# Kernel optimization log

Hardware: AMD Instinct MI355X
Metric: run time of the kernel (lower is better)

The kernel has to match this reference:

```python
import jax, jax.numpy as jnp
import numpy as np

B, T, C = 2, 2048, 1024
H = 16
HD = C // H  # head_dim = 64
SCALE = HD ** -0.5

def setup_inputs() -> dict:
    key = jax.random.key(0)
    ks = jax.random.split(key, 5)
    s = 1.0 / np.sqrt(C)
    return {
        "x": jax.random.normal(ks[0], (B, T, C), dtype=jnp.float32),
        "Wq": jax.random.normal(ks[1], (C, C), dtype=jnp.float32) * s,
        "Wk": jax.random.normal(ks[2], (C, C), dtype=jnp.float32) * s,
        "Wv": jax.random.normal(ks[3], (C, C), dtype=jnp.float32) * s,
        "Wp": jax.random.normal(ks[4], (C, C), dtype=jnp.float32) * s,
        "bp": jnp.zeros((C,), dtype=jnp.float32),
    }

def reference(x, Wq, Wk, Wv, Wp, bp):
    b, t, c = x.shape
    # QKV projections (no bias, qkv_bias=False) -> [B,T,H,HD]
    q = (x @ Wq).reshape(b, t, H, HD)
    k = (x @ Wk).reshape(b, t, H, HD)
    v = (x @ Wv).reshape(b, t, H, HD)
    # scores [B,H,T,T]
    scores = jnp.einsum("bqhd,bkhd->bhqk", q, k) * SCALE
    causal = jnp.tril(jnp.ones((t, t), dtype=bool))
    scores = jnp.where(causal, scores, -jnp.inf)
    attn = jax.nn.softmax(scores, axis=-1)  # dropout = identity (eval mode)
    out = jnp.einsum("bhqk,bkhd->bqhd", attn, v).reshape(b, t, c)
    return out @ Wp + bp
```

## Files before the change

### kernel.cpp

```cpp
#include <hip/hip_runtime.h>


typedef __attribute__((ext_vector_type(8))) short shortx8;
typedef __attribute__((ext_vector_type(4))) short shortx4;
typedef __attribute__((ext_vector_type(8))) unsigned short ushortx8;
typedef __attribute__((ext_vector_type(4))) float f32x4;
typedef __attribute__((ext_vector_type(16))) float f32x16;

#define MFMA16(a, b, c) __builtin_amdgcn_mfma_f32_16x16x32_bf16((a), (b), (c), 0, 0, 0)
#define MFMA32(a, b, c) __builtin_amdgcn_mfma_f32_32x32x16_bf16((a), (b), (c), 0, 0, 0)

#define SC_L2E 0.18033688011112042f

__device__ __forceinline__ unsigned short f2bf(float f) {
  union { float f; unsigned u; } v; v.f = f;
  unsigned r = v.u + 0x7fffu + ((v.u >> 16) & 1u);
  return (unsigned short)(r >> 16);
}

__device__ __forceinline__ unsigned cvtpk(float a, float b) {
  unsigned r;
  asm("v_cvt_pk_bf16_f32 %0, %1, %2" : "=v"(r) : "v"(a), "v"(b));
  return r;
}

__device__ __forceinline__ float fexp2(float x) {
#if __has_builtin(__builtin_amdgcn_exp2f)
  return __builtin_amdgcn_exp2f(x);
#else
  return exp2f(x);
#endif
}

__device__ __forceinline__ void gload16(const void* g, void* l) {
  __builtin_amdgcn_global_load_lds(
      (const __attribute__((address_space(1))) void*)g,
      (__attribute__((address_space(3))) void*)l, 16, 0, 0);
}

__global__ __launch_bounds__(256) void cvt_x(const float* __restrict__ x,
                                             unsigned short* __restrict__ xb, int n4) {
  int i = blockIdx.x * 256 + threadIdx.x;
  if (i < n4) {
    float4 v = ((const float4*)x)[i];
    unsigned short* o = xb + (size_t)i * 4;
    o[0] = f2bf(v.x); o[1] = f2bf(v.y); o[2] = f2bf(v.z); o[3] = f2bf(v.w);
  }
}

__global__ __launch_bounds__(256) void transpose_w4(
    const float* __restrict__ Wq, const float* __restrict__ Wk,
    const float* __restrict__ Wv, const float* __restrict__ Wp,
    unsigned short* __restrict__ wqkvT, unsigned short* __restrict__ wpT) {
  __shared__ float tile[32][33];
  const int zi = blockIdx.z;
  const float* src = (zi == 0) ? Wq : (zi == 1) ? Wk : (zi == 2) ? Wv : Wp;
  unsigned short* dst = (zi == 3) ? wpT : wqkvT + (size_t)zi * 1048576;
  const int bx = blockIdx.x * 32, by = blockIdx.y * 32;
  const int tx = threadIdx.x & 31, ty = threadIdx.x >> 5;
  #pragma unroll
  for (int i = 0; i < 32; i += 8)
    tile[ty + i][tx] = src[(size_t)(by + ty + i) * 1024 + bx + tx];
  __syncthreads();
  #pragma unroll
  for (int i = 0; i < 32; i += 8)
    dst[(size_t)(bx + ty + i) * 1024 + by + tx] = f2bf(tile[tx][ty + i]);
}

__global__ __launch_bounds__(256) void gemm_bt(
    const unsigned short* __restrict__ A, const unsigned short* __restrict__ BT,
    unsigned short* __restrict__ Cb, float* __restrict__ Cf,
    const float* __restrict__ bias, int M, int N, int K,
    float qscale, int scale_cols, unsigned short* __restrict__ vTo) {
  __shared__ unsigned short As[2][128 * 32];
  __shared__ unsigned short Bs[2][128 * 32];
  const int tid = threadIdx.x;
  const int lane = tid & 63, w = tid >> 6;
  const int wr = w >> 1, wc = w & 1;
  const int brow = blockIdx.y << 7, bcol = blockIdx.x << 7;

  f32x4 z = {0.f, 0.f, 0.f, 0.f};
  f32x4 acc[4][4];
  #pragma unroll
  for (int m = 0; m < 4; ++m)
    #pragma unroll
    for (int n = 0; n < 4; ++n) acc[m][n] = z;

  const int srow = tid >> 2;
  const int scol = (tid & 3) << 3;
  const unsigned short* Ap = A + (size_t)(brow + srow) * K + scol;
  const unsigned short* Bp = BT + (size_t)(bcol + srow) * K + scol;
  const size_t rowK64 = (size_t)64 * K;

  #define GSTAGE(k0_, bi_)                                   \
    do {                                                     \
      unsigned short* AsW = &As[bi_][w * 512];               \
      unsigned short* BsW = &Bs[bi_][w * 512];               \
      gload16(Ap + (k0_), AsW);                              \
      gload16(Ap + rowK64 + (k0_), AsW + 2048);              \
      gload16(Bp + (k0_), BsW);                              \
      gload16(Bp + rowK64 + (k0_), BsW + 2048);              \
    } while (0)

  const int koff = (lane >> 4) << 3;
  const int ar = (wr << 6) + (lane & 15);
  const int br = (wc << 6) + (lane & 15);
  const int nt = K >> 5;
  int bufi = 0;
  GSTAGE(0, 0);
  for (int t = 0; t < nt; ++t) {
    if (t + 1 < nt) {
      GSTAGE((size_t)(t + 1) << 5, bufi ^ 1);
      asm volatile("s_waitcnt vmcnt(4)" ::: "memory");
    } else {
      asm volatile("s_waitcnt vmcnt(0)" ::: "memory");
    }
    __builtin_amdgcn_sched_barrier(0);
    __builtin_amdgcn_s_barrier();
    __builtin_amdgcn_sched_barrier(0);
    shortx8 af[4], bf[4];
    #pragma unroll
    for (int m = 0; m < 4; ++m) af[m] = *(const shortx8*)&As[bufi][(ar + m * 16) * 32 + koff];
    #pragma unroll
    for (int n = 0; n < 4; ++n) bf[n] = *(const shortx8*)&Bs[bufi][(br + n * 16) * 32 + koff];
    #pragma unroll
    for (int m = 0; m < 4; ++m)
      #pragma unroll
      for (int n = 0; n < 4; ++n) acc[m][n] = MFMA16(af[m], bf[n], acc[m][n]);
    asm volatile("s_waitcnt lgkmcnt(0)" ::: "memory");
    __builtin_amdgcn_sched_barrier(0);
    __builtin_amdgcn_s_barrier();
    __builtin_amdgcn_sched_barrier(0);
    bufi ^= 1;
  }
  #undef GSTAGE

  const int r0 = (lane >> 4) << 2;
  const int c0 = lane & 15;
  if (Cb) {
    if (vTo && bcol >= 2048) {
      #pragma unroll
      for (int m = 0; m < 4; ++m)
        #pragma unroll
        for (int n = 0; n < 4; ++n) {
          const int dp = bcol - 2048 + (wc << 6) + n * 16 + c0;
          const size_t rowb = brow + (wr << 6) + m * 16 + r0;
          uint2 u;
          u.x = cvtpk(acc[m][n][0], acc[m][n][1]);
          u.y = cvtpk(acc[m][n][2], acc[m][n][3]);
          *(uint2*)&vTo[(size_t)dp * 4096 + rowb] = u;
        }
    } else {
      #pragma unroll
      for (int m = 0; m < 4; ++m)
        #pragma unroll
        for (int n = 0; n < 4; ++n)
          #pragma unroll
          for (int j = 0; j < 4; ++j) {
            const size_t row = brow + (wr << 6) + m * 16 + r0 + j;
            const size_t col = bcol + (wc << 6) + n * 16 + c0;
            float v = acc[m][n][j];
            if ((int)col < scale_cols) v *= qscale;
            Cb[row * N + col] = f2bf(v);
          }
    }
  } else {
    #pragma unroll
    for (int m = 0; m < 4; ++m)
      #pragma unroll
      for (int n = 0; n < 4; ++n)
        #pragma unroll
        for (int j = 0; j < 4; ++j) {
          const size_t row = brow + (wr << 6) + m * 16 + r0 + j;
          const size_t col = bcol + (wc << 6) + n * 16 + c0;
          Cf[row * N + col] = acc[m][n][j] + bias[col];
        }
  }
}


__global__ __launch_bounds__(128, 4) void attn_fwd(
    const unsigned short* __restrict__ qkv, const unsigned short* __restrict__ vT,
    unsigned short* __restrict__ att) {
  __shared__ unsigned short sh[2][4096];

  const int tid = threadIdx.x;
  const int lane = tid & 63;
  const int p = tid >> 6;
  const int stream = blockIdx.x;
  const int h = stream & 15, b = stream >> 4;
  const int qb = 63 - (int)blockIdx.y;
  const int ql = lane & 31;
  const int hi = lane >> 5;
  const int q = qb * 32 + ql;

  shortx8 qf[4];
  {
    const unsigned short* qp = qkv + ((size_t)(b * 2048 + q)) * 3072 + h * 64 + 8 * hi;
    #pragma unroll
    for (int kc = 0; kc < 4; ++kc) qf[kc] = *(const shortx8*)(qp + 16 * kc);
  }

  f32x16 z16;
  #pragma unroll
  for (int i = 0; i < 16; ++i) z16[i] = 0.f;
  f32x16 accO0 = z16, accO1 = z16;
  float m_run = -__builtin_inff(), l_run = 0.f;

  const unsigned short* kb[4];
  const unsigned short* vb[4];
  #pragma unroll
  for (int i = 0; i < 4; ++i) {
    const int krow = 8 * i + (lane >> 3);
    const int kcl = (lane & 7) ^ (((krow >> 1) ^ (krow >> 4)) & 7);
    kb[i] = qkv + ((size_t)(b * 2048 + krow)) * 3072 + 1024 + h * 64 + 8 * kcl;
    const int vrow = 16 * i + (lane >> 2);
    const int vcl = (lane & 3) ^ (((vrow >> 1) ^ (vrow >> 3)) & 3);
    vb[i] = vT + ((size_t)(h * 64 + vrow)) * 4096 + b * 2048 + 8 * vcl;
  }
  const int rs8 = ((ql >> 1) ^ (ql >> 4)) & 7;
  const int rs4 = ((ql >> 1) ^ (ql >> 3)) & 3;

  unsigned short* Kl = &sh[p][0];
  unsigned short* Vl = &sh[p][2048];

  #define STAGE(t_)                                                        \
    do {                                                                   \
      _Pragma("unroll")                                                    \
      for (int i = 0; i < 4; ++i) {                                        \
        gload16(kb[i] + (size_t)(t_) * 32 * 3072, Kl + i * 512);           \
        gload16(vb[i] + (t_) * 32, Vl + i * 512);                          \
      }                                                                    \
    } while (0)

  if (p <= qb) STAGE(p);
  for (int t = p; t <= qb; t += 2) {
    asm volatile("s_waitcnt vmcnt(0)" ::: "memory");
    __builtin_amdgcn_sched_barrier(0);

    shortx8 kf[4];
    #pragma unroll
    for (int kc = 0; kc < 4; ++kc)
      kf[kc] = *(const shortx8*)&Kl[ql * 64 + 8 * ((2 * kc + hi) ^ rs8)];
    shortx8 vf[2][2];
    #pragma unroll
    for (int dh = 0; dh < 2; ++dh)
      #pragma unroll
      for (int ks = 0; ks < 2; ++ks)
        vf[dh][ks] = *(const shortx8*)&Vl[(32 * dh + ql) * 32 + 8 * ((2 * ks + hi) ^ rs4)];
    asm volatile("s_waitcnt lgkmcnt(0)" ::: "memory");
    __builtin_amdgcn_sched_barrier(0);

    if (t + 2 <= qb) STAGE(t + 2);

    __builtin_amdgcn_s_setprio(1);
    f32x16 s = z16;
    #pragma unroll
    for (int kc = 0; kc < 4; ++kc) s = MFMA32(kf[kc], qf[kc], s);
    __builtin_amdgcn_s_setprio(0);

    if (t == qb) {
      #pragma unroll
      for (int r = 0; r < 16; ++r) {
        const int kvl = (r & 3) + 8 * (r >> 2) + 4 * hi;
        if (kvl > ql) s[r] = -__builtin_inff();
      }
    }

    float m8[8], m4[4];
    #pragma unroll
    for (int i = 0; i < 8; ++i) m8[i] = fmaxf(s[2 * i], s[2 * i + 1]);
    #pragma unroll
    for (int i = 0; i < 4; ++i) m4[i] = fmaxf(m8[2 * i], m8[2 * i + 1]);
    float mx = fmaxf(fmaxf(m4[0], m4[1]), fmaxf(m4[2], m4[3]));
    mx = fmaxf(mx, __shfl_xor(mx, 32));

    if (!__all(mx <= m_run + 8.0f)) {
      const float nm = fmaxf(m_run, mx);
      const float alpha = fexp2(m_run - nm);
      l_run *= alpha;
      #pragma unroll
      for (int r = 0; r < 16; ++r) { accO0[r] *= alpha; accO1[r] *= alpha; }
      m_run = nm;
    }

    #pragma unroll
    for (int r = 0; r < 16; ++r) s[r] = fexp2(s[r] - m_run);
    float a8[8], a4[4];
    #pragma unroll
    for (int i = 0; i < 8; ++i) a8[i] = s[2 * i] + s[2 * i + 1];
    #pragma unroll
    for (int i = 0; i < 4; ++i) a4[i] = a8[2 * i] + a8[2 * i + 1];
    float rsum = (a4[0] + a4[1]) + (a4[2] + a4[3]);
    rsum += __shfl_xor(rsum, 32);
    l_run += rsum;

    unsigned wv[8], xv[8];
    #pragma unroll
    for (int i = 0; i < 8; ++i) wv[i] = cvtpk(s[2 * i], s[2 * i + 1]);
    #pragma unroll
    for (int i = 0; i < 8; ++i) xv[i] = __shfl_xor(wv[i], 32);
    __builtin_amdgcn_s_setprio(1);
    #pragma unroll
    for (int ss = 0; ss < 2; ++ss) {
      union { unsigned u[4]; shortx8 s8; } pb;
      pb.u[0] = hi ? xv[4 * ss + 2] : wv[4 * ss];
      pb.u[1] = hi ? xv[4 * ss + 3] : wv[4 * ss + 1];
      pb.u[2] = hi ? wv[4 * ss + 2] : xv[4 * ss];
      pb.u[3] = hi ? wv[4 * ss + 3] : xv[4 * ss + 1];
      accO0 = MFMA32(vf[0][ss], pb.s8, accO0);
      accO1 = MFMA32(vf[1][ss], pb.s8, accO1);
    }
    __builtin_amdgcn_s_setprio(0);
  }
  #undef STAGE

  __syncthreads();
  float* mb = (float*)&sh[0][0];
  float* ml = mb + 2048;
  if (p == 1) {
    #pragma unroll
    for (int rg = 0; rg < 4; ++rg) {
      f32x4 v0 = {accO0[4 * rg], accO0[4 * rg + 1], accO0[4 * rg + 2], accO0[4 * rg + 3]};
      f32x4 v1 = {accO1[4 * rg], accO1[4 * rg + 1], accO1[4 * rg + 2], accO1[4 * rg + 3]};
      *(f32x4*)&mb[(rg * 64 + lane) * 4] = v0;
      *(f32x4*)&mb[((4 + rg) * 64 + lane) * 4] = v1;
    }
    ml[lane] = m_run;
    ml[64 + lane] = l_run;
  }
  __syncthreads();
  if (p == 0) {
    const float m1 = ml[lane], l1 = ml[64 + lane];
    const float mf = fmaxf(m_run, m1);
    const float a0 = fexp2(m_run - mf);
    const float a1 = fexp2(m1 - mf);
    const float inv = 1.f / (l_run * a0 + l1 * a1);
    unsigned short* op = att + ((size_t)(b * 2048 + q)) * 1024 + h * 64;
    #pragma unroll
    for (int rq = 0; rq < 4; ++rq) {
      f32x4 p0 = *(const f32x4*)&mb[(rq * 64 + lane) * 4];
      f32x4 p1 = *(const f32x4*)&mb[((4 + rq) * 64 + lane) * 4];
      shortx4 o0, o1;
      #pragma unroll
      for (int j = 0; j < 4; ++j) {
        o0[j] = (short)f2bf((accO0[4 * rq + j] * a0 + p0[j] * a1) * inv);
        o1[j] = (short)f2bf((accO1[4 * rq + j] * a0 + p1[j] * a1) * inv);
      }
      *(shortx4*)&op[8 * rq + 4 * hi] = o0;
      *(shortx4*)&op[32 + 8 * rq + 4 * hi] = o1;
    }
  }
}

extern "C" void kernel_launch(void* const* d_in, const int* in_sizes, int n_in,
                              void* d_out, int out_size, void* d_ws, size_t ws_size,
                              hipStream_t stream) {
  const float* x  = (const float*)d_in[0];
  const float* Wq = (const float*)d_in[1];
  const float* Wk = (const float*)d_in[2];
  const float* Wv = (const float*)d_in[3];
  const float* Wp = (const float*)d_in[4];
  const float* bp = (const float*)d_in[5];

  char* ws = (char*)d_ws;
  unsigned short* xb    = (unsigned short*)(ws);
  unsigned short* wqkvT = (unsigned short*)(ws + (size_t)8  * 1048576);
  unsigned short* wpT   = (unsigned short*)(ws + (size_t)14 * 1048576);
  unsigned short* qkv   = (unsigned short*)(ws + (size_t)16 * 1048576);
  unsigned short* vT    = (unsigned short*)(ws + (size_t)40 * 1048576);
  unsigned short* att   = (unsigned short*)(ws + (size_t)48 * 1048576);

  cvt_x<<<dim3(4096), dim3(256), 0, stream>>>(x, xb, 1048576);
  transpose_w4<<<dim3(32, 32, 4), dim3(256), 0, stream>>>(Wq, Wk, Wv, Wp, wqkvT, wpT);
  gemm_bt<<<dim3(24, 32), dim3(256), 0, stream>>>(xb, wqkvT, qkv, nullptr, nullptr,
                                                  4096, 3072, 1024, SC_L2E, 1024, vT);
  attn_fwd<<<dim3(32, 64), dim3(128), 0, stream>>>(qkv, vT, att);
  gemm_bt<<<dim3(8, 32), dim3(256), 0, stream>>>(att, wpT, nullptr, (float*)d_out, bp,
                                                 4096, 1024, 1024, 0.f, 0, nullptr);
}
```

Measured before the change: 114.3 us.

## Split attention KV loop across four waves with tree merge of partial softmax states

Each attention block now uses four waves instead of two, each handling every fourth 32-key tile, with LDS doubled to hold per-wave staging buffers. The partial outputs and running max/sum are combined in two rounds of LDS dump-and-merge, with guards for waves that processed no tiles. This shortens the serial KV loop per block, especially for late query blocks, at the cost of more LDS, extra synchronization and merge work, and fewer blocks resident per CU.

```diff
diff --git a/kernel.cpp b/kernel.cpp
--- a/kernel.cpp
+++ b/kernel.cpp
@@ -179,10 +179,10 @@
 }
 
 
-__global__ __launch_bounds__(128, 4) void attn_fwd(
+__global__ __launch_bounds__(256, 5) void attn_fwd(
     const unsigned short* __restrict__ qkv, const unsigned short* __restrict__ vT,
     unsigned short* __restrict__ att) {
-  __shared__ unsigned short sh[2][4096];
+  __shared__ unsigned short sh[4][4096];
 
   const int tid = threadIdx.x;
   const int lane = tid & 63;
@@ -234,7 +234,7 @@
     } while (0)
 
   if (p <= qb) STAGE(p);
-  for (int t = p; t <= qb; t += 2) {
+  for (int t = p; t <= qb; t += 4) {
     asm volatile("s_waitcnt vmcnt(0)" ::: "memory");
     __builtin_amdgcn_sched_barrier(0);
 
@@ -251,7 +251,7 @@
     asm volatile("s_waitcnt lgkmcnt(0)" ::: "memory");
     __builtin_amdgcn_sched_barrier(0);
 
-    if (t + 2 <= qb) STAGE(t + 2);
+    if (t + 4 <= qb) STAGE(t + 4);
 
     __builtin_amdgcn_s_setprio(1);
     f32x16 s = z16;
@@ -315,42 +315,73 @@
   }
   #undef STAGE
 
+  float* fb = (float*)&sh[0][0];
+  #define DUMP(slot_)                                                          \
+    do {                                                                       \
+      float* ob = fb + (slot_) * 2048;                                         \
+      _Pragma("unroll")                                                        \
+      for (int rg = 0; rg < 4; ++rg) {                                         \
+        f32x4 v0 = {accO0[4 * rg], accO0[4 * rg + 1],                          \
+                    accO0[4 * rg + 2], accO0[4 * rg + 3]};                     \
+        f32x4 v1 = {accO1[4 * rg], accO1[4 * rg + 1],                          \
+                    accO1[4 * rg + 2], accO1[4 * rg + 3]};                     \
+        *(f32x4*)&ob[(rg * 64 + lane) * 4] = v0;                               \
+        *(f32x4*)&ob[((4 + rg) * 64 + lane) * 4] = v1;                         \
+      }                                                                        \
+      fb[4096 + (slot_) * 128 + lane] = m_run;                                 \
+      fb[4096 + (slot_) * 128 + 64 + lane] = l_run;                            \
+    } while (0)
+  #define MERGE(slot_)                                                         \
+    do {                                                                       \
+      const float m2 = fb[4096 + (slot_) * 128 + lane];                        \
+      const float l2 = fb[4096 + (slot_) * 128 + 64 + lane];                   \
+      if (m2 != -__builtin_inff()) {                                           \
+        float* ob = fb + (slot_) * 2048;                                       \
+        const float mf = fmaxf(m_run, m2);                                     \
+        const float a1 = fexp2(m_run - mf);                                    \
+        const float a2 = fexp2(m2 - mf);                                       \
+        _Pragma("unroll")                                                      \
+        for (int rg = 0; rg < 4; ++rg) {                                       \
+          f32x4 p0 = *(const f32x4*)&ob[(rg * 64 + lane) * 4];                 \
+          f32x4 p1 = *(const f32x4*)&ob[((4 + rg) * 64 + lane) * 4];           \
+          _Pragma("unroll")                                                    \
+          for (int j = 0; j < 4; ++j) {                                        \
+            accO0[4 * rg + j] = accO0[4 * rg + j] * a1 + p0[j] * a2;           \
+            accO1[4 * rg + j] = accO1[4 * rg + j] * a1 + p1[j] * a2;           \
+          }                                                                    \
+        }                                                                      \
+        l_run = l_run * a1 + l2 * a2;                                          \
+        m_run = mf;                                                            \
+      }                                                                        \
+    } while (0)
+
   __syncthreads();
-  float* mb = (float*)&sh[0][0];
-  float* ml = mb + 2048;
-  if (p == 1) {
-    #pragma unroll
-    for (int rg = 0; rg < 4; ++rg) {
-      f32x4 v0 = {accO0[4 * rg], accO0[4 * rg + 1], accO0[4 * rg + 2], accO0[4 * rg + 3]};
-      f32x4 v1 = {accO1[4 * rg], accO1[4 * rg + 1], accO1[4 * rg + 2], accO1[4 * rg + 3]};
-      *(f32x4*)&mb[(rg * 64 + lane) * 4] = v0;
-      *(f32x4*)&mb[((4 + rg) * 64 + lane) * 4] = v1;
-    }
-    ml[lane] = m_run;
-    ml[64 + lane] = l_run;
-  }
+  if (p == 1) DUMP(0);
+  if (p == 3) DUMP(1);
+  __syncthreads();
+  if (p == 0) MERGE(0);
+  if (p == 2) MERGE(1);
+  __syncthreads();
+  if (p == 2) DUMP(0);
   __syncthreads();
   if (p == 0) {
-    const float m1 = ml[lane], l1 = ml[64 + lane];
-    const float mf = fmaxf(m_run, m1);
-    const float a0 = fexp2(m_run - mf);
-    const float a1 = fexp2(m1 - mf);
-    const float inv = 1.f / (l_run * a0 + l1 * a1);
+    MERGE(0);
+    const float inv = 1.f / l_run;
     unsigned short* op = att + ((size_t)(b * 2048 + q)) * 1024 + h * 64;
     #pragma unroll
     for (int rq = 0; rq < 4; ++rq) {
-      f32x4 p0 = *(const f32x4*)&mb[(rq * 64 + lane) * 4];
-      f32x4 p1 = *(const f32x4*)&mb[((4 + rq) * 64 + lane) * 4];
       shortx4 o0, o1;
       #pragma unroll
       for (int j = 0; j < 4; ++j) {
-        o0[j] = (short)f2bf((accO0[4 * rq + j] * a0 + p0[j] * a1) * inv);
-        o1[j] = (short)f2bf((accO1[4 * rq + j] * a0 + p1[j] * a1) * inv);
+        o0[j] = (short)f2bf(accO0[4 * rq + j] * inv);
+        o1[j] = (short)f2bf(accO1[4 * rq + j] * inv);
       }
       *(shortx4*)&op[8 * rq + 4 * hi] = o0;
       *(shortx4*)&op[32 + 8 * rq + 4 * hi] = o1;
     }
   }
+  #undef DUMP
+  #undef MERGE
 }
 
 extern "C" void kernel_launch(void* const* d_in, const int* in_sizes, int n_in,
@@ -375,7 +406,7 @@
   transpose_w4<<<dim3(32, 32, 4), dim3(256), 0, stream>>>(Wq, Wk, Wv, Wp, wqkvT, wpT);
   gemm_bt<<<dim3(24, 32), dim3(256), 0, stream>>>(xb, wqkvT, qkv, nullptr, nullptr,
                                                   4096, 3072, 1024, SC_L2E, 1024, vT);
-  attn_fwd<<<dim3(32, 64), dim3(128), 0, stream>>>(qkv, vT, att);
+  attn_fwd<<<dim3(32, 64), dim3(256), 0, stream>>>(qkv, vT, att);
   gemm_bt<<<dim3(8, 32), dim3(256), 0, stream>>>(att, wpT, nullptr, (float*)d_out, bp,
                                                  4096, 1024, 1024, 0.f, 0, nullptr);
 }
```

After: 170.8 us. +49.4%, slower.
